# Kernel tuning notes

Hardware: AMD Instinct MI355X
Metric: run time of the kernel (lower is better)

The kernel has to match this reference:

```python
import jax, jax.numpy as jnp
import numpy as np

N, M, K, D = 65536, 131072, 8, 64
TAU = 0.3
EPS = 1e-6

def setup_inputs() -> dict:
    key = jax.random.key(0)
    ks = jax.random.split(key, 16)
    s = 0.05
    return {
        "f_pts": jax.random.normal(ks[0], (N, D), jnp.float32),
        "pts": jax.random.uniform(ks[1], (N, 3), jnp.float32) * 10.0,
        "z_latent": jax.random.normal(ks[2], (M, D), jnp.float32) * 0.1,
        "centers": jax.random.uniform(ks[3], (M, 3), jnp.float32) * 10.0,
        "cand_idx": jax.random.randint(ks[4], (N, K), 0, M),
        "sim_w1": jax.random.normal(ks[5], (2 * D + 3, 64), jnp.float32) * s,
        "sim_b1": jnp.zeros((64,), jnp.float32),
        "sim_w2": jax.random.normal(ks[6], (64, 1), jnp.float32) * s,
        "sim_b2": jnp.zeros((1,), jnp.float32),
        "gate_w1": jax.random.normal(ks[7], (2 * D, D), jnp.float32) * s,
        "gate_b1": jnp.zeros((D,), jnp.float32),
        "gate_w2": jax.random.normal(ks[8], (D, 1), jnp.float32) * s,
        "gate_b2": jnp.zeros((1,), jnp.float32),
        "W_ih": jax.random.normal(ks[9], (3 * D, D), jnp.float32) * s,
        "W_hh": jax.random.normal(ks[10], (3 * D, D), jnp.float32) * s,
        "b_ih": jnp.zeros((3 * D,), jnp.float32),
        "b_hh": jnp.zeros((3 * D,), jnp.float32),
    }

def _forward(f_pts, pts, z_latent, centers, sim_w1, sim_b1, sim_w2, sim_b2,
             gate_w1, gate_b1, gate_w2, gate_b2, W_ih, W_hh, b_ih, b_hh, cand_idx):
    n, k = cand_idx.shape
    m, d = z_latent.shape
    # --- gather voxel latents / centers for each (point, candidate) pair ---
    z_c = z_latent[cand_idx]                         # (N,K,D)
    delta = pts[:, None, :] - centers[cand_idx]      # (N,K,3)
    f_b = jnp.broadcast_to(f_pts[:, None, :], (n, k, d))
    # --- similarity MLP ---
    x = jnp.concatenate([f_b, z_c, delta], axis=-1)  # (N,K,2D+3)
    h = jax.nn.relu(x @ sim_w1 + sim_b1)
    sim = (h @ sim_w2 + sim_b2)[..., 0]              # (N,K)
    # --- low-temperature top-K routing weights over candidates ---
    w = jax.nn.softmax(sim / TAU, axis=-1)           # (N,K)
    # --- scatter weighted point features to voxels ---
    flat_idx = cand_idx.reshape(-1)                  # (N*K,)
    contrib = (w[..., None] * f_pts[:, None, :]).reshape(-1, d)
    msg = jax.ops.segment_sum(contrib, flat_idx, num_segments=m)     # (M,D)
    wsum = jax.ops.segment_sum(w.reshape(-1), flat_idx, num_segments=m)
    msg = msg / (wsum[:, None] + EPS)                # normalized voxel message
    # --- per-voxel gate ---
    g_in = jnp.concatenate([z_latent, msg], axis=-1)
    gate = jax.nn.sigmoid(jax.nn.relu(g_in @ gate_w1 + gate_b1) @ gate_w2 + gate_b2)  # (M,1)
    # --- GRUCell (torch layout: rows ordered r,z,n) ---
    gi = msg @ W_ih.T + b_ih
    gh = z_latent @ W_hh.T + b_hh
    i_r, i_z, i_n = jnp.split(gi, 3, axis=-1)
    h_r, h_z, h_n = jnp.split(gh, 3, axis=-1)
    r = jax.nn.sigmoid(i_r + h_r)
    zg = jax.nn.sigmoid(i_z + h_z)
    nn_ = jnp.tanh(i_n + r * h_n)
    h_new = (1.0 - zg) * nn_ + zg * z_latent
    # gated latent update
    return z_latent + gate * (h_new - z_latent)

def reference(f_pts, pts, z_latent, centers, cand_idx, sim_w1, sim_b1, sim_w2, sim_b2,
              gate_w1, gate_b1, gate_w2, gate_b2, W_ih, W_hh, b_ih, b_hh):
    return _forward(f_pts, pts, z_latent, centers, sim_w1, sim_b1, sim_w2, sim_b2,
                    gate_w1, gate_b1, gate_w2, gate_b2, W_ih, W_hh, b_ih, b_hh, cand_idx)
```

## Files before the change

### kernel.cpp

```cpp
#include <hip/hip_runtime.h>
#include <hip/hip_fp16.h>
#include <math.h>


typedef short bf16x8 __attribute__((ext_vector_type(8)));
typedef unsigned short u16x8 __attribute__((ext_vector_type(8)));
typedef float f32x4 __attribute__((ext_vector_type(4)));
#define MFMA __builtin_amdgcn_mfma_f32_16x16x32_bf16
#define CAP 32

__device__ __forceinline__ short f2bf(float f) {
  unsigned u = __float_as_uint(f);
  unsigned r = (u + 0x7FFFu + ((u >> 16) & 1u)) >> 16;
  return (short)r;
}

__device__ __forceinline__ float bf2f(unsigned short h) {
  return __uint_as_float(((unsigned)h) << 16);
}

__device__ __forceinline__ float sigm(float x) { return 1.0f / (1.0f + __expf(-x)); }

__global__ __launch_bounds__(256) void prep_kernel(
    const float* __restrict__ z, const float* __restrict__ f,
    const float* __restrict__ sim_w1, const float* __restrict__ sim_b1,
    unsigned short* __restrict__ zbf, unsigned short* __restrict__ fbf,
    unsigned short* __restrict__ HBt, int* __restrict__ cursor,
    short* __restrict__ bfZ, int M)
{
  long tid = (long)blockIdx.x * 256 + threadIdx.x;
  long nthr = (long)gridDim.x * 256;

  for (long i = tid; i < M; i += nthr) cursor[i] = 0;

  long nz = (long)M * 64;
  for (long i = tid * 8; i < nz; i += nthr * 8) {
    float4 a = *(const float4*)&z[i];
    float4 b4 = *(const float4*)&z[i + 4];
    u16x8 o;
    o[0] = (unsigned short)f2bf(a.x);  o[1] = (unsigned short)f2bf(a.y);
    o[2] = (unsigned short)f2bf(a.z);  o[3] = (unsigned short)f2bf(a.w);
    o[4] = (unsigned short)f2bf(b4.x); o[5] = (unsigned short)f2bf(b4.y);
    o[6] = (unsigned short)f2bf(b4.z); o[7] = (unsigned short)f2bf(b4.w);
    *(u16x8*)&zbf[i] = o;
  }

  if (blockIdx.x == gridDim.x - 1 && threadIdx.x < 64) {
    int lane = threadIdx.x;
    int lr = lane & 15, lg = lane >> 4;
#pragma unroll
    for (int ct = 0; ct < 4; ++ct)
#pragma unroll
      for (int kt = 0; kt < 3; ++kt) {
        bf16x8 b;
#pragma unroll
        for (int e = 0; e < 8; ++e) {
          int k = kt * 32 + lg * 8 + e;
          float v = (k < 67) ? sim_w1[(64 + k) * 64 + ct * 16 + lr] : 0.0f;
          b[e] = f2bf(v);
        }
        *(bf16x8*)&bfZ[(ct * 3 + kt) * 512 + lane * 8] = b;
      }
  }

  if (blockIdx.x < 1024) {
    int wave = blockIdx.x * 4 + (threadIdx.x >> 6);
    int lane = threadIdx.x & 63;
    int lr = lane & 15, lg = lane >> 4;
    int n0 = wave * 16;

    bf16x8 bf[8];
#pragma unroll
    for (int ct = 0; ct < 4; ++ct)
#pragma unroll
      for (int kt = 0; kt < 2; ++kt) {
        bf16x8 bb;
#pragma unroll
        for (int e = 0; e < 8; ++e)
          bb[e] = f2bf(sim_w1[(kt * 32 + lg * 8 + e) * 64 + ct * 16 + lr]);
        bf[ct * 2 + kt] = bb;
      }

    bf16x8 a[2];
#pragma unroll
    for (int kt = 0; kt < 2; ++kt) {
      const float* src = &f[(long)(n0 + lr) * 64 + kt * 32 + lg * 8];
      float4 v0 = *(const float4*)src;
      float4 v1 = *(const float4*)(src + 4);
      bf16x8 t;
      t[0] = f2bf(v0.x); t[1] = f2bf(v0.y); t[2] = f2bf(v0.z); t[3] = f2bf(v0.w);
      t[4] = f2bf(v1.x); t[5] = f2bf(v1.y); t[6] = f2bf(v1.z); t[7] = f2bf(v1.w);
      a[kt] = t;
    }
    *(bf16x8*)&fbf[(long)(n0 + lr) * 64 + lg * 8] = a[0];
    *(bf16x8*)&fbf[(long)(n0 + lr) * 64 + 32 + lg * 8] = a[1];

    f32x4 acc[4] = {{0,0,0,0},{0,0,0,0},{0,0,0,0},{0,0,0,0}};
#pragma unroll
    for (int ct = 0; ct < 4; ++ct) {
      acc[ct] = MFMA(a[0], bf[ct * 2 + 0], acc[ct], 0, 0, 0);
      acc[ct] = MFMA(a[1], bf[ct * 2 + 1], acc[ct], 0, 0, 0);
    }
    float b10 = sim_b1[lr], b11 = sim_b1[16 + lr];
    float b12 = sim_b1[32 + lr], b13 = sim_b1[48 + lr];
#pragma unroll
    for (int e = 0; e < 4; ++e) {
      unsigned lo = (unsigned)(unsigned short)f2bf(acc[0][e] + b10)
                  | ((unsigned)(unsigned short)f2bf(acc[1][e] + b11) << 16);
      unsigned hi = (unsigned)(unsigned short)f2bf(acc[2][e] + b12)
                  | ((unsigned)(unsigned short)f2bf(acc[3][e] + b13) << 16);
      *(uint2*)&HBt[(long)(n0 + lg * 4 + e) * 64 + lr * 4] = make_uint2(lo, hi);
    }
  }
}

#define TPW 4
__global__ __launch_bounds__(256) void pair_kernel(
    const float* __restrict__ pts, const unsigned short* __restrict__ zbf,
    const float* __restrict__ centers, const int* __restrict__ cand_idx,
    const float* __restrict__ sim_w2, const short* __restrict__ bfZ,
    const unsigned short* __restrict__ HBt,
    int* __restrict__ cursor, unsigned* __restrict__ rec)
{
  int wave = (blockIdx.x * 256 + threadIdx.x) >> 6;
  int lane = threadIdx.x & 63;
  int lr = lane & 15, lg = lane >> 4;

  int call = cand_idx[wave * 64 + lane];
  int slot = atomicAdd(&cursor[call], 1);

  bf16x8 b[12];
#pragma unroll
  for (int i = 0; i < 12; ++i) b[i] = *(const bf16x8*)&bfZ[i * 512 + lane * 8];
  float w2c[4];
#pragma unroll
  for (int ct = 0; ct < 4; ++ct) w2c[ct] = sim_w2[ct * 16 + lr];

  int c[TPW];
  bf16x8 a0[TPW], a1[TPW], ad[TPW];
  uint2 h2[TPW];
#pragma unroll
  for (int t = 0; t < TPW; ++t) {
    c[t] = __shfl(call, t * 16 + lr, 64);
    a0[t] = *(const bf16x8*)&zbf[(long)c[t] * 64 + lg * 8];
    a1[t] = *(const bf16x8*)&zbf[(long)c[t] * 64 + 32 + lg * 8];
    h2[t] = *(const uint2*)&HBt[((long)(wave * TPW + t) * 2 + (lg >> 1)) * 64 + lr * 4];
    bf16x8 tt = {0, 0, 0, 0, 0, 0, 0, 0};
    if (lg == 0) {
      int n = (wave * TPW + t) * 2 + (lr >> 3);
      tt[0] = f2bf(pts[n * 3 + 0] - centers[c[t] * 3 + 0]);
      tt[1] = f2bf(pts[n * 3 + 1] - centers[c[t] * 3 + 1]);
      tt[2] = f2bf(pts[n * 3 + 2] - centers[c[t] * 3 + 2]);
    }
    ad[t] = tt;
  }

  f32x4 part[TPW];
#pragma unroll
  for (int t = 0; t < TPW; ++t) {
    f32x4 acc[4] = {{0,0,0,0},{0,0,0,0},{0,0,0,0},{0,0,0,0}};
#pragma unroll
    for (int ct = 0; ct < 4; ++ct) {
      acc[ct] = MFMA(a0[t], b[ct * 3 + 0], acc[ct], 0, 0, 0);
      acc[ct] = MFMA(a1[t], b[ct * 3 + 1], acc[ct], 0, 0, 0);
      acc[ct] = MFMA(ad[t], b[ct * 3 + 2], acc[ct], 0, 0, 0);
    }
    float hb[4];
    hb[0] = bf2f((unsigned short)(h2[t].x));
    hb[1] = bf2f((unsigned short)(h2[t].x >> 16));
    hb[2] = bf2f((unsigned short)(h2[t].y));
    hb[3] = bf2f((unsigned short)(h2[t].y >> 16));
    f32x4 p = {0.f, 0.f, 0.f, 0.f};
#pragma unroll
    for (int ct = 0; ct < 4; ++ct)
#pragma unroll
      for (int e = 0; e < 4; ++e)
        p[e] = fmaf(fmaxf(acc[ct][e] + hb[ct], 0.0f), w2c[ct], p[e]);
    part[t] = p;
  }

  float wrow[TPW];
#pragma unroll
  for (int t = 0; t < TPW; ++t) {
    f32x4 p = part[t];
#pragma unroll
    for (int m = 1; m <= 8; m <<= 1)
#pragma unroll
      for (int e = 0; e < 4; ++e) p[e] += __shfl_xor(p[e], m, 64);
    float other[4];
#pragma unroll
    for (int e = 0; e < 4; ++e) other[e] = __shfl_xor(p[e], 16, 64);
    float mx = p[0];
#pragma unroll
    for (int e = 1; e < 4; ++e) mx = fmaxf(mx, p[e]);
#pragma unroll
    for (int e = 0; e < 4; ++e) mx = fmaxf(mx, other[e]);
    float ex[4], se = 0.f, so = 0.f;
#pragma unroll
    for (int e = 0; e < 4; ++e) {
      ex[e] = __expf((p[e] - mx) * (1.0f / 0.3f));
      se += ex[e];
      so += __expf((other[e] - mx) * (1.0f / 0.3f));
    }
    float inv = 1.0f / (se + so);
    int srcl = (lane >> 2) << 4;
    float t0 = __shfl(ex[0] * inv, srcl, 64);
    float t1 = __shfl(ex[1] * inv, srcl, 64);
    float t2 = __shfl(ex[2] * inv, srcl, 64);
    float t3 = __shfl(ex[3] * inv, srcl, 64);
    int esel = lane & 3;
    wrow[t] = esel == 0 ? t0 : esel == 1 ? t1 : esel == 2 ? t2 : t3;
  }

  float v0 = __shfl(wrow[0], lr, 64);
  float v1 = __shfl(wrow[1], lr, 64);
  float v2 = __shfl(wrow[2], lr, 64);
  float v3 = __shfl(wrow[3], lr, 64);
  float wv = lg == 0 ? v0 : lg == 1 ? v1 : lg == 2 ? v2 : v3;

  if (slot < CAP) {
    int n_pt = wave * 8 + 2 * lg + (lr >> 3);
    unsigned short wh = __half_as_ushort(__float2half(wv));
    rec[(long)call * CAP + slot] = ((unsigned)n_pt << 16) | (unsigned)wh;
  }
}

#define GST 136
#define WST 72

__global__ __launch_bounds__(512)
__attribute__((amdgpu_waves_per_eu(2, 2)))
void stage2(
    const unsigned short* __restrict__ zbf,
    const float* __restrict__ gate_w1, const float* __restrict__ gate_b1,
    const float* __restrict__ gate_w2, const float* __restrict__ gate_b2,
    const float* __restrict__ W_ih, const float* __restrict__ W_hh,
    const float* __restrict__ b_ih, const float* __restrict__ b_hh,
    const unsigned* __restrict__ rec, const int* __restrict__ cursor,
    const unsigned short* __restrict__ fbf,
    float* __restrict__ out, int ntiles)
{
  __shared__ short G1t[64 * GST];
  __shared__ short Wih_l[192 * WST];
  __shared__ short Whh_l[192 * WST];
  __shared__ float gb1s[64], gw2s[64], bihs[192], bhhs[192];
  __shared__ float gb2s;

  int t = threadIdx.x;
  for (int s = t; s < 64 * 128; s += 512) {
    int j = s & 63, k = s >> 6;
    G1t[j * GST + k] = f2bf(gate_w1[s]);
  }
  for (int s = t; s < 192 * 64; s += 512) {
    int j = s >> 6, k = s & 63;
    Wih_l[j * WST + k] = f2bf(W_ih[s]);
    Whh_l[j * WST + k] = f2bf(W_hh[s]);
  }
  if (t < 64) { gb1s[t] = gate_b1[t]; gw2s[t] = gate_w2[t]; }
  if (t < 192) { bihs[t] = b_ih[t]; bhhs[t] = b_hh[t]; }
  if (t == 0) gb2s = gate_b2[0];
  __syncthreads();

  int wid = t >> 6, lane = t & 63;
  int lr = lane & 15, lg = lane >> 4;

#pragma unroll 1
  for (int tile = blockIdx.x; tile < ntiles; tile += gridDim.x) {
    int rowbase = tile * 128 + wid * 16;
    int myrow = rowbase + lr;
    long abase = (long)myrow * 64;
    bf16x8 a0 = *(const bf16x8*)&zbf[abase + lg * 8];
    bf16x8 a1 = *(const bf16x8*)&zbf[abase + 32 + lg * 8];

    int cnt = cursor[myrow];
    cnt = cnt < CAP ? cnt : CAP;
    const unsigned* rp = &rec[(long)myrow * CAP];
    float accA[8], accB[8];
#pragma unroll
    for (int k = 0; k < 8; ++k) { accA[k] = 0.f; accB[k] = 0.f; }
    float ws = 0.f;
#pragma unroll 1
    for (int i0 = 0; i0 < cnt; i0 += 4) {
      uint4 r4 = *(const uint4*)&rp[i0];
#pragma unroll
      for (int j = 0; j < 4; ++j) {
        unsigned r = j == 0 ? r4.x : j == 1 ? r4.y : j == 2 ? r4.z : r4.w;
        if (i0 + j < cnt) {
          float w = __half2float(__ushort_as_half((unsigned short)(r & 0xffffu)));
          int n = r >> 16;
          ws += w;
          u16x8 fA = *(const u16x8*)&fbf[(long)n * 64 + lg * 8];
          u16x8 fB = *(const u16x8*)&fbf[(long)n * 64 + 32 + lg * 8];
#pragma unroll
          for (int k = 0; k < 8; ++k) {
            accA[k] = fmaf(w, bf2f(fA[k]), accA[k]);
            accB[k] = fmaf(w, bf2f(fB[k]), accB[k]);
          }
        }
      }
    }
    float minv = 1.0f / (ws + 1e-6f);
    bf16x8 a2, a3;
#pragma unroll
    for (int k = 0; k < 8; ++k) {
      a2[k] = f2bf(accA[k] * minv);
      a3[k] = f2bf(accB[k] * minv);
    }

    f32x4 usum = {0.f, 0.f, 0.f, 0.f};
#pragma unroll 1
    for (int ct = 0; ct < 4; ++ct) {
      f32x4 au = {0, 0, 0, 0};
      au = MFMA(a0, *(const bf16x8*)&G1t[(ct * 16 + lr) * GST +  0 + lg * 8], au, 0, 0, 0);
      au = MFMA(a1, *(const bf16x8*)&G1t[(ct * 16 + lr) * GST + 32 + lg * 8], au, 0, 0, 0);
      au = MFMA(a2, *(const bf16x8*)&G1t[(ct * 16 + lr) * GST + 64 + lg * 8], au, 0, 0, 0);
      au = MFMA(a3, *(const bf16x8*)&G1t[(ct * 16 + lr) * GST + 96 + lg * 8], au, 0, 0, 0);
      int c = ct * 16 + lr;
#pragma unroll
      for (int e = 0; e < 4; ++e)
        usum[e] += fmaxf(au[e] + gb1s[c], 0.0f) * gw2s[c];
    }
#pragma unroll
    for (int m = 1; m <= 8; m <<= 1)
#pragma unroll
      for (int e = 0; e < 4; ++e) {
        float v = usum[e];
        usum[e] = v + __shfl_xor(v, m, 64);
      }
    float gate[4];
#pragma unroll
    for (int e = 0; e < 4; ++e) gate[e] = sigm(usum[e] + gb2s);

#pragma unroll 1
    for (int ct = 0; ct < 4; ++ct) {
      f32x4 air = {0,0,0,0}, aiz = {0,0,0,0}, ain = {0,0,0,0};
      f32x4 ahr = {0,0,0,0}, ahz = {0,0,0,0}, ahn = {0,0,0,0};
#pragma unroll
      for (int k2 = 0; k2 < 2; ++k2) {
        bf16x8 amg = k2 ? a3 : a2;
        bf16x8 az_ = k2 ? a1 : a0;
        int ko = k2 * 32 + lg * 8;
        air = MFMA(amg, *(const bf16x8*)&Wih_l[(      ct * 16 + lr) * WST + ko], air, 0, 0, 0);
        aiz = MFMA(amg, *(const bf16x8*)&Wih_l[( 64 + ct * 16 + lr) * WST + ko], aiz, 0, 0, 0);
        ain = MFMA(amg, *(const bf16x8*)&Wih_l[(128 + ct * 16 + lr) * WST + ko], ain, 0, 0, 0);
        ahr = MFMA(az_, *(const bf16x8*)&Whh_l[(      ct * 16 + lr) * WST + ko], ahr, 0, 0, 0);
        ahz = MFMA(az_, *(const bf16x8*)&Whh_l[( 64 + ct * 16 + lr) * WST + ko], ahz, 0, 0, 0);
        ahn = MFMA(az_, *(const bf16x8*)&Whh_l[(128 + ct * 16 + lr) * WST + ko], ahn, 0, 0, 0);
      }
      int c = ct * 16 + lr;
#pragma unroll
      for (int e = 0; e < 4; ++e) {
        float zv = bf2f(zbf[(long)(rowbase + lg * 4 + e) * 64 + c]);
        float rr = sigm(air[e] + bihs[c] + ahr[e] + bhhs[c]);
        float zg = sigm(aiz[e] + bihs[64 + c] + ahz[e] + bhhs[64 + c]);
        float nn = tanhf(ain[e] + bihs[128 + c] + rr * (ahn[e] + bhhs[128 + c]));
        float hnew = (1.0f - zg) * nn + zg * zv;
        out[(long)(rowbase + lg * 4 + e) * 64 + c] = zv + gate[e] * (hnew - zv);
      }
    }
  }
}

extern "C" void kernel_launch(void* const* d_in, const int* in_sizes, int n_in,
                              void* d_out, int out_size, void* d_ws, size_t ws_size,
                              hipStream_t stream) {
  const float* f_pts   = (const float*)d_in[0];
  const float* pts     = (const float*)d_in[1];
  const float* z_lat   = (const float*)d_in[2];
  const float* centers = (const float*)d_in[3];
  const int*   cand    = (const int*)d_in[4];
  const float* sim_w1  = (const float*)d_in[5];
  const float* sim_b1  = (const float*)d_in[6];
  const float* sim_w2  = (const float*)d_in[7];
  const float* gate_w1 = (const float*)d_in[9];
  const float* gate_b1 = (const float*)d_in[10];
  const float* gate_w2 = (const float*)d_in[11];
  const float* gate_b2 = (const float*)d_in[12];
  const float* W_ih    = (const float*)d_in[13];
  const float* W_hh    = (const float*)d_in[14];
  const float* b_ih    = (const float*)d_in[15];
  const float* b_hh    = (const float*)d_in[16];

  int N = in_sizes[0] / 64;
  int M = in_sizes[2] / 64;

  int* cursor = (int*)d_ws;
  unsigned* rec = (unsigned*)(cursor + M);
  unsigned short* zbf = (unsigned short*)(rec + (size_t)M * CAP);
  unsigned short* fbf = zbf + (size_t)M * 64;
  unsigned short* HBt = fbf + (size_t)N * 64;
  short* bfZ = (short*)(HBt + (size_t)N * 64);

  prep_kernel<<<2048, 256, 0, stream>>>(z_lat, f_pts, sim_w1, sim_b1,
                                        zbf, fbf, HBt, cursor, bfZ, M);

  int nwaves = (N * 8) / (16 * TPW);
  pair_kernel<<<nwaves / 4, 256, 0, stream>>>(pts, zbf, centers, cand,
                                              sim_w2, bfZ, HBt, cursor, rec);

  int ntiles = M / 128;
  stage2<<<512, 512, 0, stream>>>(zbf, gate_w1, gate_b1, gate_w2, gate_b2,
                                  W_ih, W_hh, b_ih, b_hh, rec, cursor, fbf,
                                  (float*)d_out, ntiles);
}
```

Measured before the change: 112.0 us.

## Split voxel message gather out of stage2 into a separate high-occupancy kernel

Moves the per-voxel weighted gather of point features out of the LDS-heavy, two-waves-per-EU stage2 kernel into a new light kernel. Four threads handle each voxel row, and the normalised message is written as bf16 into the space of the voxel's own record buffer, which stage2 then loads directly. The aim is to hide the scattered feature-load latency with much higher occupancy than stage2 allows. In exchange it adds a kernel launch and a write-then-read round trip of the message buffer. The in-place aliasing of rec is only safe because the four threads of a row run in lockstep within one wave.

New measurement: 110.5 us. No clear change (-1.4%).

```diff
diff --git a/kernel.cpp b/kernel.cpp
--- a/kernel.cpp
+++ b/kernel.cpp
@@ -225,6 +225,55 @@
   }
 }
 
+__global__ __launch_bounds__(256) void gather_kernel(
+    const unsigned* __restrict__ rec, const int* __restrict__ cursor,
+    const unsigned short* __restrict__ fbf, unsigned short* __restrict__ msg_bf,
+    int mvox)
+{
+  int tid = blockIdx.x * 256 + threadIdx.x;
+  int row = tid >> 2, seg = tid & 3;
+  if (row >= mvox) return;
+
+  int cnt = cursor[row];
+  cnt = cnt < CAP ? cnt : CAP;
+  const unsigned* rp = &rec[(long)row * CAP];
+
+  float acc[16];
+#pragma unroll
+  for (int j = 0; j < 16; ++j) acc[j] = 0.f;
+  float ws = 0.f;
+
+  for (int i0 = 0; i0 < cnt; i0 += 4) {
+    uint4 r4 = *(const uint4*)&rp[i0];
+    unsigned rr0 = r4.x, rr1 = r4.y, rr2 = r4.z, rr3 = r4.w;
+#pragma unroll
+    for (int j = 0; j < 4; ++j) {
+      unsigned r = j == 0 ? rr0 : j == 1 ? rr1 : j == 2 ? rr2 : rr3;
+      if (i0 + j < cnt) {
+        float w = __half2float(__ushort_as_half((unsigned short)(r & 0xffffu)));
+        int n = r >> 16;
+        ws += w;
+        const u16x8* fp = (const u16x8*)&fbf[(long)n * 64 + seg * 16];
+        u16x8 f0 = fp[0], f1 = fp[1];
+#pragma unroll
+        for (int k = 0; k < 8; ++k) {
+          acc[k]     = fmaf(w, bf2f(f0[k]), acc[k]);
+          acc[8 + k] = fmaf(w, bf2f(f1[k]), acc[8 + k]);
+        }
+      }
+    }
+  }
+  float inv = 1.0f / (ws + 1e-6f);
+  u16x8 o0, o1;
+#pragma unroll
+  for (int j = 0; j < 8; ++j) {
+    o0[j] = (unsigned short)f2bf(acc[j] * inv);
+    o1[j] = (unsigned short)f2bf(acc[8 + j] * inv);
+  }
+  *(u16x8*)&msg_bf[(long)row * 64 + seg * 16] = o0;
+  *(u16x8*)&msg_bf[(long)row * 64 + seg * 16 + 8] = o1;
+}
+
 #define GST 136
 #define WST 72
 
@@ -236,8 +285,7 @@
     const float* __restrict__ gate_w2, const float* __restrict__ gate_b2,
     const float* __restrict__ W_ih, const float* __restrict__ W_hh,
     const float* __restrict__ b_ih, const float* __restrict__ b_hh,
-    const unsigned* __restrict__ rec, const int* __restrict__ cursor,
-    const unsigned short* __restrict__ fbf,
+    const unsigned short* __restrict__ msg_bf,
     float* __restrict__ out, int ntiles)
 {
   __shared__ short G1t[64 * GST];
@@ -267,45 +315,11 @@
 #pragma unroll 1
   for (int tile = blockIdx.x; tile < ntiles; tile += gridDim.x) {
     int rowbase = tile * 128 + wid * 16;
-    int myrow = rowbase + lr;
-    long abase = (long)myrow * 64;
+    long abase = (long)(rowbase + lr) * 64;
     bf16x8 a0 = *(const bf16x8*)&zbf[abase + lg * 8];
     bf16x8 a1 = *(const bf16x8*)&zbf[abase + 32 + lg * 8];
-
-    int cnt = cursor[myrow];
-    cnt = cnt < CAP ? cnt : CAP;
-    const unsigned* rp = &rec[(long)myrow * CAP];
-    float accA[8], accB[8];
-#pragma unroll
-    for (int k = 0; k < 8; ++k) { accA[k] = 0.f; accB[k] = 0.f; }
-    float ws = 0.f;
-#pragma unroll 1
-    for (int i0 = 0; i0 < cnt; i0 += 4) {
-      uint4 r4 = *(const uint4*)&rp[i0];
-#pragma unroll
-      for (int j = 0; j < 4; ++j) {
-        unsigned r = j == 0 ? r4.x : j == 1 ? r4.y : j == 2 ? r4.z : r4.w;
-        if (i0 + j < cnt) {
-          float w = __half2float(__ushort_as_half((unsigned short)(r & 0xffffu)));
-          int n = r >> 16;
-          ws += w;
-          u16x8 fA = *(const u16x8*)&fbf[(long)n * 64 + lg * 8];
-          u16x8 fB = *(const u16x8*)&fbf[(long)n * 64 + 32 + lg * 8];
-#pragma unroll
-          for (int k = 0; k < 8; ++k) {
-            accA[k] = fmaf(w, bf2f(fA[k]), accA[k]);
-            accB[k] = fmaf(w, bf2f(fB[k]), accB[k]);
-          }
-        }
-      }
-    }
-    float minv = 1.0f / (ws + 1e-6f);
-    bf16x8 a2, a3;
-#pragma unroll
-    for (int k = 0; k < 8; ++k) {
-      a2[k] = f2bf(accA[k] * minv);
-      a3[k] = f2bf(accB[k] * minv);
-    }
+    bf16x8 a2 = *(const bf16x8*)&msg_bf[abase + lg * 8];
+    bf16x8 a3 = *(const bf16x8*)&msg_bf[abase + 32 + lg * 8];
 
     f32x4 usum = {0.f, 0.f, 0.f, 0.f};
 #pragma unroll 1
@@ -386,6 +400,7 @@
 
   int* cursor = (int*)d_ws;
   unsigned* rec = (unsigned*)(cursor + M);
+  unsigned short* msg_bf = (unsigned short*)rec;
   unsigned short* zbf = (unsigned short*)(rec + (size_t)M * CAP);
   unsigned short* fbf = zbf + (size_t)M * 64;
   unsigned short* HBt = fbf + (size_t)N * 64;
@@ -398,8 +413,10 @@
   pair_kernel<<<nwaves / 4, 256, 0, stream>>>(pts, zbf, centers, cand,
                                               sim_w2, bfZ, HBt, cursor, rec);
 
+  gather_kernel<<<(M * 4) / 256, 256, 0, stream>>>(rec, cursor, fbf, msg_bf, M);
+
   int ntiles = M / 128;
   stage2<<<512, 512, 0, stream>>>(zbf, gate_w1, gate_b1, gate_w2, gate_b2,
-                                  W_ih, W_hh, b_ih, b_hh, rec, cursor, fbf,
+                                  W_ih, W_hh, b_ih, b_hh, msg_bf,
                                   (float*)d_out, ntiles);
 }
```
